# Performance work log

Hardware: AMD Instinct MI355X
Metric: run time of the kernel (lower is better)

The kernel has to match this reference:

```python
import jax, jax.numpy as jnp
import numpy as np

B, N, D, L = 64, 2047, 512, 4
T = D + 1        # token_dim = d + 1
H = 512          # hidden_dim
LN_EPS = 1e-5
ATTN_EPS = 1e-6


def setup_inputs() -> dict:
    key = jax.random.key(0)
    ks = jax.random.split(key, 10)
    s = 0.01  # matches xavier_uniform_ gain=0.01 small-init magnitude
    return dict(
        xs=jax.random.normal(ks[0], (B, N, D), jnp.float32),
        ys=jax.random.normal(ks[1], (B, N), jnp.float32),
        query_x=jax.random.normal(ks[2], (B, 1, D), jnp.float32),
        Wq=jax.random.normal(ks[3], (L, H, T), jnp.float32) * s,
        Wk=jax.random.normal(ks[4], (L, H, T), jnp.float32) * s,
        Wv=jax.random.normal(ks[5], (L, T, T), jnp.float32) * s,
        Wo=jax.random.normal(ks[6], (L, T, T), jnp.float32) * s,
        ln1_w=jnp.ones((L, T), jnp.float32),
        ln1_b=jnp.zeros((L, T), jnp.float32),
        ln2_w=jnp.ones((L, T), jnp.float32),
        ln2_b=jnp.zeros((L, T), jnp.float32),
        scale=jnp.ones((L,), jnp.float32),
        pred_w=jax.random.normal(ks[7], (1, T), jnp.float32) * 0.02,
    )


def _ln(x, w, b):
    m = jnp.mean(x, axis=-1, keepdims=True)
    v = jnp.var(x, axis=-1, keepdims=True)
    return (x - m) * jax.lax.rsqrt(v + LN_EPS) * w + b


def _l2norm(x):
    n = jnp.sqrt(jnp.sum(x * x, axis=-1, keepdims=True))
    return x / jnp.maximum(n, 1e-12)


def _forward(xs, ys, query_x, Wq, Wk, Wv, Wo, ln1_w, ln1_b, ln2_w, ln2_b, scale, pred_w):
    b = xs.shape[0]
    train_tokens = jnp.concatenate([xs, ys[..., None]], axis=-1)          # [B,N,T]
    query_token = jnp.concatenate([query_x, jnp.zeros((b, 1, 1), xs.dtype)], axis=-1)
    tokens = jnp.concatenate([train_tokens, query_token], axis=1)          # [B,N+1,T]

    def step(tok, p):
        wq, wk, wv, wo, w1, b1, w2, b2, sc = p
        x = _ln(tok, w1, b1)
        Q = jnp.einsum('bnt,ht->bnh', x, wq)
        K = jnp.einsum('bnt,ht->bnh', x, wk)
        V = jnp.einsum('bnt,ut->bnu', x, wv)
        Q = _l2norm(Q)
        K = _l2norm(K)
        s = jax.nn.softplus(sc)
        Qp = (jax.nn.elu(Q) + 1.0) * s
        Kp = jax.nn.elu(K) + 1.0
        KV = jnp.einsum('bnh,bnu->bhu', Kp, V)      # [B,H,T]
        Ksum = jnp.sum(Kp, axis=1)                  # [B,H]
        denom = jnp.einsum('bnh,bh->bn', Qp, Ksum)  # [B,N+1]
        attn = jnp.einsum('bnh,bhu->bnu', Qp, KV) / (denom[..., None] + ATTN_EPS)
        out = jnp.einsum('bnu,tu->bnt', attn, wo) * 0.1 + tok
        return _ln(out, w2, b2), None

    tokens, _ = jax.lax.scan(step, tokens, (Wq, Wk, Wv, Wo, ln1_w, ln1_b, ln2_w, ln2_b, scale))
    q_out = tokens[:, -1, :]                        # [B,T]
    return jnp.einsum('bt,ot->bo', q_out, pred_w)[..., 0]  # [B]


def reference(xs, ys, query_x, Wq, Wk, Wv, Wo, ln1_w, ln1_b, ln2_w, ln2_b, scale, pred_w):
    return _forward(xs, ys, query_x, Wq, Wk, Wv, Wo, ln1_w, ln1_b, ln2_w, ln2_b, scale, pred_w)
```

## Files before the change

kernel.cpp:

```cpp
#include <hip/hip_runtime.h>
#include <cstdint>
#include <cstddef>


typedef unsigned short u16;
typedef float f32x4 __attribute__((ext_vector_type(4)));
typedef unsigned short u16x8 __attribute__((ext_vector_type(8)));

#define P 576
#define NQK 1664
#define VTROWS 514
#define KVLD 640

__device__ __forceinline__ float bf2f(u16 s) {
    union { unsigned u; float f; } v; v.u = ((unsigned)s) << 16; return v.f;
}
__device__ __forceinline__ u16 f2bf(float f) {
    union { float f; unsigned u; } v; v.f = f;
    unsigned r = v.u + 0x7FFF + ((v.u >> 16) & 1);
    return (u16)(r >> 16);
}
__device__ __forceinline__ float wredsum(float v) {
#pragma unroll
    for (int o = 32; o > 0; o >>= 1) v += __shfl_xor(v, o, 64);
    return v;
}
__device__ __forceinline__ f32x4 mfma_16x16x32_bf16(u16x8 a, u16x8 b, f32x4 c) {
    asm volatile("v_mfma_f32_16x16x32_bf16 %0, %1, %2, %0"
                 : "+v"(c) : "v"(a), "v"(b));
    return c;
}
__device__ __forceinline__ void gload_lds16(const u16* g, u16* l) {
    __builtin_amdgcn_global_load_lds(
        (const __attribute__((address_space(1))) void*)g,
        (__attribute__((address_space(3))) void*)l, 16, 0, 0);
}

__global__ __launch_bounds__(256) void k_build_tokens(
    const float* __restrict__ xs, const float* __restrict__ ys,
    const float* __restrict__ qx, u16* __restrict__ tok,
    float* __restrict__ meanb, float* __restrict__ rstdb)
{
    long row = (long)blockIdx.x * 4 + (threadIdx.x >> 6);
    int lane = threadIdx.x & 63;
    int b = (int)(row >> 11), n = (int)(row & 2047);
    const float* src = (n < 2047) ? xs + ((long)(b * 2047 + n)) * 512
                                  : qx + (long)b * 512;
    float4 f0 = *(const float4*)(src + lane * 8);
    float4 f1 = *(const float4*)(src + lane * 8 + 4);
    float y = (n < 2047) ? ys[(long)b * 2047 + n] : 0.f;
    float v[8] = {f0.x, f0.y, f0.z, f0.w, f1.x, f1.y, f1.z, f1.w};
    float s = 0.f, sq = 0.f;
#pragma unroll
    for (int j = 0; j < 8; j++) { s += v[j]; sq += v[j] * v[j]; }
    if (lane == 0) { s += y; sq += y * y; }
    s = wredsum(s); sq = wredsum(sq);
    u16x8 o;
#pragma unroll
    for (int j = 0; j < 8; j++) o[j] = f2bf(v[j]);
    *(u16x8*)(tok + row * P + lane * 8) = o;
    if (lane < 8) {
        u16x8 z8 = {0,0,0,0,0,0,0,0};
        if (lane == 0) z8[0] = f2bf(y);
        *(u16x8*)(tok + row * P + 512 + lane * 8) = z8;
    }
    if (lane == 0) {
        float m = s * (1.f / 513.f);
        float var = sq * (1.f / 513.f) - m * m;
        meanb[row] = m;
        rstdb[row] = 1.f / sqrtf(var + 1e-5f);
    }
}

__global__ __launch_bounds__(256) void k_prep_wcat(
    const float* __restrict__ wq, const float* __restrict__ wk,
    const float* __restrict__ wv, const float* __restrict__ ln1w,
    u16* __restrict__ wcat)
{
    long idx = (long)blockIdx.x * 256 + threadIdx.x;
    if (idx >= 4L * NQK * P) return;
    int t = (int)(idx % P);
    long rem = idx / P;
    int r = (int)(rem % NQK);
    int l = (int)(rem / NQK);
    float v = 0.f;
    if (t < 513) {
        float wsc = ln1w[l * 513 + t];
        if (r < 512)       v = wq[((long)l * 512 + r) * 513 + t] * wsc;
        else if (r < 1024) v = wk[((long)l * 512 + (r - 512)) * 513 + t] * wsc;
        else if (r < 1537) v = wv[((long)l * 513 + (r - 1024)) * 513 + t] * wsc;
    }
    wcat[idx] = f2bf(v);
}

__global__ __launch_bounds__(256) void k_prep_wo(
    const float* __restrict__ wo, u16* __restrict__ wop)
{
    long idx = (long)blockIdx.x * 256 + threadIdx.x;
    if (idx >= 4L * P * P) return;
    int u = (int)(idx % P);
    long rem = idx / P;
    int t = (int)(rem % P);
    int l = (int)(rem / P);
    float v = (t < 513 && u < 513) ? wo[((long)l * 513 + t) * 513 + u] : 0.f;
    wop[idx] = f2bf(v);
}

__global__ __launch_bounds__(256) void k_prep_sums(
    const float* __restrict__ wq, const float* __restrict__ wk,
    const float* __restrict__ wv, const float* __restrict__ ln1w,
    const float* __restrict__ ln1b, float* __restrict__ s1, float* __restrict__ s2)
{
    int id = blockIdx.x * 4 + (threadIdx.x >> 6);
    int lane = threadIdx.x & 63;
    int l = id / NQK, r = id % NQK;
    float a1 = 0.f, a2 = 0.f;
    for (int t = lane; t < 513; t += 64) {
        float wc = 0.f;
        if (r < 512)       wc = wq[((long)l * 512 + r) * 513 + t];
        else if (r < 1024) wc = wk[((long)l * 512 + (r - 512)) * 513 + t];
        else if (r < 1537) wc = wv[((long)l * 513 + (r - 1024)) * 513 + t];
        a1 += ln1w[l * 513 + t] * wc;
        a2 += ln1b[l * 513 + t] * wc;
    }
    a1 = wredsum(a1); a2 = wredsum(a2);
    if (lane == 0) { s1[id] = a1; s2[id] = a2; }
}

__global__ __launch_bounds__(256) void k_ln2(
    const u16* __restrict__ z, u16* __restrict__ tok,
    const float* __restrict__ w, const float* __restrict__ bia,
    float* __restrict__ meanb, float* __restrict__ rstdb,
    const float* __restrict__ znum, const float* __restrict__ denomb)
{
    long row = (long)blockIdx.x * 4 + (threadIdx.x >> 6);
    int lane = threadIdx.x & 63;
    const u16* zp = z + row * P;
    u16* tp = tok + row * P;
    u16x8 a0 = *(const u16x8*)(zp + lane * 8);
    float zc = 0.f;
    if (lane == 0)
        zc = 0.1f * znum[row] / (denomb[row] + 1e-6f) + bf2f(tp[512]);
    float v0[8], v1[8];
#pragma unroll
    for (int j = 0; j < 8; j++) v0[j] = bf2f(a0[j]);
#pragma unroll
    for (int j = 0; j < 8; j++) v1[j] = 0.f;
    v1[0] = zc;
    float s = 0.f, sq = 0.f;
#pragma unroll
    for (int j = 0; j < 8; j++) { s += v0[j]; sq += v0[j] * v0[j]; }
#pragma unroll
    for (int j = 0; j < 8; j++) { s += v1[j]; sq += v1[j] * v1[j]; }
    s = wredsum(s); sq = wredsum(sq);
    float mean = s * (1.f / 513.f);
    float var = sq * (1.f / 513.f) - mean * mean;
    float rstd = 1.f / sqrtf(var + 1e-5f);
    float so = 0.f, so2 = 0.f;
    u16x8 o0;
    float of0[8];
#pragma unroll
    for (int j = 0; j < 8; j++) {
        int t = lane * 8 + j;
        of0[j] = (v0[j] - mean) * rstd * w[t] + bia[t];
        so += of0[j]; so2 += of0[j] * of0[j];
        o0[j] = f2bf(of0[j]);
    }
    float of1[8];
#pragma unroll
    for (int j = 0; j < 8; j++) {
        int t = 512 + lane * 8 + j;
        float ov = 0.f;
        if (lane < 8 && t < 513) ov = (v1[j] - mean) * rstd * w[t] + bia[t];
        of1[j] = ov;
        so += ov; so2 += ov * ov;
    }
    so = wredsum(so); so2 = wredsum(so2);
    *(u16x8*)(tp + lane * 8) = o0;
    if (lane < 8) {
        u16x8 o1;
#pragma unroll
        for (int j = 0; j < 8; j++) o1[j] = f2bf(of1[j]);
        *(u16x8*)(tp + 512 + lane * 8) = o1;
    }
    if (lane == 0) {
        float m2 = so * (1.f / 513.f);
        float v2 = so2 * (1.f / 513.f) - m2 * m2;
        meanb[row] = m2;
        rstdb[row] = 1.f / sqrtf(v2 + 1e-5f);
    }
}

__global__ __launch_bounds__(256) void k_qkt(
    u16* __restrict__ qkv, u16* __restrict__ kpt,
    float* __restrict__ ksum, float* __restrict__ v512sum,
    const u16* __restrict__ vt, const float* __restrict__ scale, int l)
{
    long row0 = (long)blockIdx.x * 64;
    int b = (int)(row0 >> 11);
    int nloc = (int)(row0 & 2047);
    int tid = threadIdx.x, lane = tid & 63, w = tid >> 6;
    float s = log1pf(expf(scale[l]));
    __shared__ u16 Kp[64][520];
    __shared__ u16 T2[64 * 80];

#pragma unroll 4
    for (int i = 0; i < 16; i++) {
        int rl = w * 16 + i;
        u16* rp = qkv + (row0 + rl) * NQK;
        u16x8 q8 = *(const u16x8*)(rp + lane * 8);
        u16x8 k8 = *(const u16x8*)(rp + 512 + lane * 8);
        float qf[8], kf[8];
        float sq = 0.f, sk = 0.f;
#pragma unroll
        for (int j = 0; j < 8; j++) { qf[j] = bf2f(q8[j]); sq += qf[j] * qf[j]; }
#pragma unroll
        for (int j = 0; j < 8; j++) { kf[j] = bf2f(k8[j]); sk += kf[j] * kf[j]; }
        sq = wredsum(sq); sk = wredsum(sk);
        float rnq = 1.f / fmaxf(sqrtf(sq), 1e-12f);
        float rnk = 1.f / fmaxf(sqrtf(sk), 1e-12f);
        u16x8 o, kk;
#pragma unroll
        for (int j = 0; j < 8; j++) {
            float q = qf[j] * rnq;
            float qp = (q > 0.f) ? (q + 1.f) : expf(q);
            o[j] = f2bf(qp * s);
            float kv = kf[j] * rnk;
            kv = (kv > 0.f) ? (kv + 1.f) : expf(kv);
            kk[j] = f2bf(kv);
        }
        *(u16x8*)(rp + lane * 8) = o;
        *(u16x8*)&Kp[rl][lane * 8] = kk;
    }
    __syncthreads();

    const u16* vrow = vt + ((long)b * VTROWS + 512) * 2048 + nloc + (tid & 3) * 16;
    u16x8 va = *(const u16x8*)vrow;
    u16x8 vb = *(const u16x8*)(vrow + 8);
    float vf[16];
#pragma unroll
    for (int j = 0; j < 8; j++) { vf[j] = bf2f(va[j]); vf[8 + j] = bf2f(vb[j]); }

    int r = tid >> 2;
    int c0 = (tid & 3) * 16;
    for (int ct = 0; ct < 8; ct++) {
        u16x8 a = *(const u16x8*)&Kp[r][ct * 64 + c0];
        u16x8 d = *(const u16x8*)&Kp[r][ct * 64 + c0 + 8];
#pragma unroll
        for (int j = 0; j < 8; j++) T2[(c0 + j) * 80 + r] = a[j];
#pragma unroll
        for (int j = 0; j < 8; j++) T2[(c0 + 8 + j) * 80 + r] = d[j];
        __syncthreads();
        u16x8 w0 = *(const u16x8*)&T2[r * 80 + c0];
        u16x8 w1 = *(const u16x8*)&T2[r * 80 + c0 + 8];
        u16* dst = kpt + ((long)(b * 512 + ct * 64 + r)) * 2048 + nloc + c0;
        *(u16x8*)dst = w0;
        *(u16x8*)(dst + 8) = w1;
        float part = 0.f, p2 = 0.f;
#pragma unroll
        for (int j = 0; j < 8; j++) {
            float k0 = bf2f(w0[j]), k1 = bf2f(w1[j]);
            part += k0 + k1;
            p2 += k0 * vf[j] + k1 * vf[8 + j];
        }
        part += __shfl_xor(part, 1, 64);
        part += __shfl_xor(part, 2, 64);
        p2 += __shfl_xor(p2, 1, 64);
        p2 += __shfl_xor(p2, 2, 64);
        if ((tid & 3) == 0) {
            atomicAdd(&ksum[(long)b * 512 + ct * 64 + r], part);
            atomicAdd(&v512sum[(long)b * 512 + ct * 64 + r], p2);
        }
        __syncthreads();
    }
}

__global__ __launch_bounds__(512) void k_v512(
    const float* __restrict__ v512sum, u16* __restrict__ kvh)
{
    int b = blockIdx.x, h = threadIdx.x;
    kvh[((long)b * 512 + h) * KVLD + 512] = f2bf(v512sum[(long)b * 512 + h]);
}

__global__ __launch_bounds__(256) void k_denom(
    const u16* __restrict__ qkv, const float* __restrict__ ksum,
    const u16* __restrict__ w2t, float* __restrict__ denom,
    float* __restrict__ znum)
{
    long row = (long)blockIdx.x * 4 + (threadIdx.x >> 6);
    int lane = threadIdx.x & 63;
    int b = (int)(row >> 11);
    u16x8 q = *(const u16x8*)(qkv + row * NQK + lane * 8);
    const float* ks = ksum + (long)b * 512 + lane * 8;
    u16x8 w8 = *(const u16x8*)(w2t + (long)b * 576 * 512 + 512 * 512 + lane * 8);
    float acc = 0.f, acc2 = 0.f;
#pragma unroll
    for (int j = 0; j < 8; j++) {
        float qf = bf2f(q[j]);
        acc += qf * ks[j];
        acc2 += qf * bf2f(w8[j]);
    }
    acc = wredsum(acc);
    acc2 = wredsum(acc2);
    if (lane == 0) { denom[row] = acc; znum[row] = acc2; }
}

__global__ void k_predict(const u16* __restrict__ tok, const float* __restrict__ pw,
                          float* __restrict__ out)
{
    int b = blockIdx.x;
    int lane = threadIdx.x;
    const u16* rp = tok + ((long)b * 2048 + 2047) * P;
    float acc = 0.f;
    for (int t = lane; t < 513; t += 64) acc += bf2f(rp[t]) * pw[t];
    acc = wredsum(acc);
    if (lane == 0) out[b] = acc;
}

__global__ __launch_bounds__(256) void k_gemm_bt(
    const u16* __restrict__ A, const u16* __restrict__ Bt, u16* __restrict__ C,
    int M, int N, int K, int lda, int ldb, int ldc,
    long sA, long sB, long sC,
    const float* __restrict__ aux1, const float* __restrict__ aux2,
    const float* __restrict__ aux3, const float* __restrict__ aux4,
    long sAux, const u16* __restrict__ Res,
    float cscale, int mode, int r1, int padw,
    int ntm, int ntn, int nbz,
    u16* __restrict__ VT, int vtbase)
{
    int G = ntm * ntn * nbz;
    int id = blockIdx.x;
    int lin = (id & 7) * (G >> 3) + (id >> 3);
    int per = ntm * ntn;
    int bz = lin / per;
    int rem = lin - bz * per;
    int mt = rem / ntn;
    int nt = rem - mt * ntn;
    int m0 = mt * 128, n0 = nt * 128;

    A += (long)bz * sA; Bt += (long)bz * sB; C += (long)bz * sC;
    int tid = threadIdx.x, lane = tid & 63, w = tid >> 6;
    int wr = w >> 1, wc = w & 1;
    __shared__ u16 ldsbuf[2 * 128 * 64];
    u16* Als = ldsbuf;
    u16* Bls = ldsbuf + 128 * 64;
    __shared__ float auxR0[128], auxR1[128], auxA1[128];
    __shared__ float auxC0[128], auxC1[128], auxB1[128];

    if (tid < 128) {
        int gr = m0 + tid; if (gr >= M) gr = M - 1;
        float r0v = cscale, r1v = 0.f, a1v = 0.f;
        if (mode == 1) {
            const float* d1 = aux1 + (long)bz * sAux;
            r0v = cscale / (d1[gr] + 1e-6f);
        } else if (mode == 3) { r0v = aux1[gr]; r1v = aux2[gr]; }
        if (r1) a1v = bf2f(A[(long)gr * lda + K]);
        auxR0[tid] = r0v; auxR1[tid] = r1v; auxA1[tid] = a1v;
    } else {
        int t = tid - 128;
        int gc = n0 + t; if (gc >= N) gc = N - 1;
        float c0v = 0.f, c1v = 0.f, b1v = 0.f;
        if (mode == 3) { c0v = aux3[gc]; c1v = aux4[gc]; }
        if (r1) b1v = bf2f(Bt[(long)gc * ldb + K]);
        auxC0[t] = c0v; auxC1[t] = c1v; auxB1[t] = b1v;
    }

    f32x4 acc[4][4];
#pragma unroll
    for (int m = 0; m < 4; m++)
#pragma unroll
        for (int n = 0; n < 4; n++) { acc[m][n][0]=0.f; acc[m][n][1]=0.f; acc[m][n][2]=0.f; acc[m][n][3]=0.f; }

    int srow = lane >> 3;
    int scol = (lane & 7) * 8;
    int scolsw = scol ^ (srow << 3);
    int swz = (lane & 7) << 3;

    for (int k0 = 0; k0 < K; k0 += 64) {
#pragma unroll
        for (int i = 0; i < 4; i++) {
            int rt = (w * 4 + i) * 8 + srow;
            int gr = m0 + rt; gr = (gr < M) ? gr : (M - 1);
            gload_lds16(A + (long)gr * lda + k0 + scolsw, &Als[(w * 4 + i) * 512]);
        }
#pragma unroll
        for (int i = 0; i < 4; i++) {
            int rt = (w * 4 + i) * 8 + srow;
            int gc = n0 + rt; gc = (gc < N) ? gc : (N - 1);
            gload_lds16(Bt + (long)gc * ldb + k0 + scolsw, &Bls[(w * 4 + i) * 512]);
        }
        __syncthreads();
#pragma unroll
        for (int ks = 0; ks < 2; ks++) {
            u16x8 af[4], bfv[4];
#pragma unroll
            for (int m = 0; m < 4; m++) {
                int row = wr * 64 + m * 16 + (lane & 15);
                af[m] = *(const u16x8*)&Als[row * 64 + ((ks * 32 + (lane >> 4) * 8) ^ swz)];
            }
#pragma unroll
            for (int n = 0; n < 4; n++) {
                int col = wc * 64 + n * 16 + (lane & 15);
                bfv[n] = *(const u16x8*)&Bls[col * 64 + ((ks * 32 + (lane >> 4) * 8) ^ swz)];
            }
#pragma unroll
            for (int m = 0; m < 4; m++)
#pragma unroll
                for (int n = 0; n < 4; n++)
                    acc[m][n] = mfma_16x16x32_bf16(af[m], bfv[n], acc[m][n]);
        }
        __syncthreads();
    }

    bool isvt = (VT != nullptr) && (n0 >= vtbase);

    if (Res) {
        const u16* Rp = Res + (long)bz * sC;
#pragma unroll
        for (int i = 0; i < 8; i++) {
            int lrow = i * 16 + (tid >> 4);
            int lcol = (tid & 15) * 8;
            long gr = m0 + lrow; if (gr > (long)M - 1) gr = M - 1;
            long gcol = (long)n0 + lcol;
            long mx = (long)ldc - 8; if (gcol > mx) gcol = mx;
            *(u16x8*)&ldsbuf[lrow * 128 + lcol] = *(const u16x8*)&Rp[gr * ldc + gcol];
        }
        __syncthreads();
    }

    asm volatile("s_nop 7\n\ts_nop 7" ::: );

    if (!isvt) {
#pragma unroll
        for (int m = 0; m < 4; m++) {
            int lrbase = wr * 64 + m * 16 + ((lane >> 4) << 2);
#pragma unroll
            for (int n = 0; n < 4; n++) {
                int lc = wc * 64 + n * 16 + (lane & 15);
                float c0v = auxC0[lc], c1v = auxC1[lc], b1v = auxB1[lc];
#pragma unroll
                for (int r = 0; r < 4; r++) {
                    int lr = lrbase + r;
                    float wv = acc[m][n][r] + auxA1[lr] * b1v;
                    float v;
                    if (mode == 3) v = auxR1[lr] * (wv - auxR0[lr] * c0v) + c1v;
                    else {
                        v = wv * auxR0[lr];
                        if (Res) v += bf2f(ldsbuf[lr * 128 + lc]);
                    }
                    ldsbuf[lr * 128 + lc] = f2bf(v);
                }
            }
        }
        __syncthreads();

        int lcol = (tid & 15) * 8;
        int gc0 = n0 + lcol;
        bool colok = padw || (gc0 + 8 <= N);
#pragma unroll
        for (int i = 0; i < 8; i++) {
            int lrow = i * 16 + (tid >> 4);
            int gr = m0 + lrow;
            if (gr < M && colok) {
                *(u16x8*)&C[(long)gr * ldc + gc0] = *(const u16x8*)&ldsbuf[lrow * 128 + lcol];
            }
        }
    } else {
        int u0 = n0 - vtbase;
        int b = m0 >> 11;
        int nloc = m0 & 2047;
#pragma unroll
        for (int m = 0; m < 4; m++) {
            int lrbase = wr * 64 + m * 16 + ((lane >> 4) << 2);
#pragma unroll
            for (int n = 0; n < 4; n++) {
                int lc = wc * 64 + n * 16 + (lane & 15);
                float c0v = auxC0[lc], c1v = auxC1[lc], b1v = auxB1[lc];
#pragma unroll
                for (int r = 0; r < 4; r++) {
                    int lr = lrbase + r;
                    float wv = acc[m][n][r] + auxA1[lr] * b1v;
                    float v = (mode == 3) ? (auxR1[lr] * (wv - auxR0[lr] * c0v) + c1v)
                                          : (wv * auxR0[lr]);
                    ldsbuf[lc * 128 + (lr ^ ((lc & 7) << 3))] = f2bf(v);
                }
            }
        }
        __syncthreads();

        int nc = (tid & 15) * 8;
        const u16x8 ones = {0x3F80,0x3F80,0x3F80,0x3F80,0x3F80,0x3F80,0x3F80,0x3F80};
#pragma unroll
        for (int i = 0; i < 8; i++) {
            int ur = i * 16 + (tid >> 4);
            int u = u0 + ur;
            if (u < VTROWS) {
                u16x8 vv;
                if (u == 513) vv = ones;
                else vv = *(const u16x8*)&ldsbuf[ur * 128 + (nc ^ ((ur & 7) << 3))];
                *(u16x8*)&VT[((long)b * VTROWS + u) * 2048 + nloc + nc] = vv;
            }
        }
    }
}

extern "C" void kernel_launch(void* const* d_in, const int* in_sizes, int n_in,
                              void* d_out, int out_size, void* d_ws, size_t ws_size,
                              hipStream_t stream)
{
    const float* xs    = (const float*)d_in[0];
    const float* ys    = (const float*)d_in[1];
    const float* qx    = (const float*)d_in[2];
    const float* Wq    = (const float*)d_in[3];
    const float* Wk    = (const float*)d_in[4];
    const float* Wv    = (const float*)d_in[5];
    const float* Wo    = (const float*)d_in[6];
    const float* ln1w  = (const float*)d_in[7];
    const float* ln1b  = (const float*)d_in[8];
    const float* ln2w  = (const float*)d_in[9];
    const float* ln2b  = (const float*)d_in[10];
    const float* scale = (const float*)d_in[11];
    const float* predw = (const float*)d_in[12];
    float* out = (float*)d_out;

    char* ws = (char*)d_ws;
    u16*   tok   = (u16*)(ws + 0L);
    u16*   buf1  = (u16*)(ws + 150994944L);
    u16*   qkv   = (u16*)(ws + 301989888L);
    u16*   kpt   = (u16*)(ws + 738197504L);
    u16*   kvh   = (u16*)(ws + 872415232L);
    float* denom = (float*)(ws + 914358272L);
    float* meanb = (float*)(ws + 914882560L);
    float* rstdb = (float*)(ws + 915406848L);
    float* ksum  = (float*)(ws + 915931136L);
    u16*   wcat  = (u16*)(ws + 916062208L);
    u16*   wop   = (u16*)(ws + 923729920L);
    float* s1    = (float*)(ws + 926384128L);
    float* s2    = (float*)(ws + 926410752L);
    float* v512s = (float*)(ws + 285736960L);
    float* znum  = (float*)(ws + 285868032L);
    u16*   w2t   = kpt;

    k_build_tokens<<<32768, 256, 0, stream>>>(xs, ys, qx, tok, meanb, rstdb);
    {
        long n1 = 4L * NQK * P;
        k_prep_wcat<<<(int)((n1 + 255) / 256), 256, 0, stream>>>(Wq, Wk, Wv, ln1w, wcat);
        long n2 = 4L * P * P;
        k_prep_wo<<<(int)((n2 + 255) / 256), 256, 0, stream>>>(Wo, wop);
        k_prep_sums<<<1664, 256, 0, stream>>>(Wq, Wk, Wv, ln1w, ln1b, s1, s2);
    }

    for (int l = 0; l < 4; l++) {
        hipMemsetAsync(ksum, 0, 64 * 512 * sizeof(float), stream);
        hipMemsetAsync(v512s, 0, 64 * 512 * sizeof(float), stream);
        k_gemm_bt<<<13312, 256, 0, stream>>>(tok, wcat + (long)l * NQK * P, qkv,
            131072, NQK, 512, P, P, NQK, 0, 0, 0,
            meanb, rstdb, s1 + l * NQK, s2 + l * NQK, 0, nullptr,
            1.f, 3, 1, 0, 1024, 13, 1,
            buf1, 1024);
        k_qkt<<<2048, 256, 0, stream>>>(qkv, kpt, ksum, v512s, buf1, scale, l);
        k_gemm_bt<<<1024, 256, 0, stream>>>(kpt, buf1, kvh,
            512, 512, 2048, 2048, 2048, KVLD,
            512L * 2048, (long)VTROWS * 2048, 512L * KVLD,
            nullptr, nullptr, nullptr, nullptr, 0, nullptr, 1.f, 0, 0, 1,
            4, 4, 64, nullptr, 1 << 30);
        k_v512<<<64, 512, 0, stream>>>(v512s, kvh);
        k_gemm_bt<<<1280, 256, 0, stream>>>(wop + (long)l * P * P, kvh, w2t,
            576, 512, 512, P, KVLD, 512,
            0, 512L * KVLD, 576L * 512,
            nullptr, nullptr, nullptr, nullptr, 0, nullptr, 1.f, 0, 1, 0,
            5, 4, 64, nullptr, 1 << 30);
        k_denom<<<32768, 256, 0, stream>>>(qkv, ksum, w2t, denom, znum);
        k_gemm_bt<<<4096, 256, 0, stream>>>(qkv, w2t, buf1,
            2048, 512, 512, NQK, 512, P,
            2048L * NQK, 576L * 512, 2048L * P,
            denom, nullptr, nullptr, nullptr, 2048, tok,
            0.1f, 1, 0, 0, 16, 4, 64, nullptr, 1 << 30);
        k_ln2<<<32768, 256, 0, stream>>>(buf1, tok, ln2w + l * 513, ln2b + l * 513,
                                         meanb, rstdb, znum, denom);
    }
    k_predict<<<64, 64, 0, stream>>>(tok, predw, out);
}
```

Baseline: 3.342 ms.

## Fuse attention-output GEMM with residual add and LayerNorm-2 in one kernel

Replaces the separate output GEMM (which wrote an intermediate buffer) and the per-row LN2 kernel with a single kernel. Each block computes a full 32-row by 512-column tile with MFMA, adds the residual, and runs both LayerNorm statistics passes in shared memory before writing tokens. This removes the intermediate buffer round-trip and one launch per layer. In exchange each block is narrow in M and reloads the whole weight tile, and uses large LDS, which may reduce occupancy.

New measurement: 3.620 ms. 8.3% more time.

```diff
diff --git a/kernel.cpp b/kernel.cpp
--- a/kernel.cpp
+++ b/kernel.cpp
@@ -127,70 +127,6 @@
     if (lane == 0) { s1[id] = a1; s2[id] = a2; }
 }
 
-__global__ __launch_bounds__(256) void k_ln2(
-    const u16* __restrict__ z, u16* __restrict__ tok,
-    const float* __restrict__ w, const float* __restrict__ bia,
-    float* __restrict__ meanb, float* __restrict__ rstdb,
-    const float* __restrict__ znum, const float* __restrict__ denomb)
-{
-    long row = (long)blockIdx.x * 4 + (threadIdx.x >> 6);
-    int lane = threadIdx.x & 63;
-    const u16* zp = z + row * P;
-    u16* tp = tok + row * P;
-    u16x8 a0 = *(const u16x8*)(zp + lane * 8);
-    float zc = 0.f;
-    if (lane == 0)
-        zc = 0.1f * znum[row] / (denomb[row] + 1e-6f) + bf2f(tp[512]);
-    float v0[8], v1[8];
-#pragma unroll
-    for (int j = 0; j < 8; j++) v0[j] = bf2f(a0[j]);
-#pragma unroll
-    for (int j = 0; j < 8; j++) v1[j] = 0.f;
-    v1[0] = zc;
-    float s = 0.f, sq = 0.f;
-#pragma unroll
-    for (int j = 0; j < 8; j++) { s += v0[j]; sq += v0[j] * v0[j]; }
-#pragma unroll
-    for (int j = 0; j < 8; j++) { s += v1[j]; sq += v1[j] * v1[j]; }
-    s = wredsum(s); sq = wredsum(sq);
-    float mean = s * (1.f / 513.f);
-    float var = sq * (1.f / 513.f) - mean * mean;
-    float rstd = 1.f / sqrtf(var + 1e-5f);
-    float so = 0.f, so2 = 0.f;
-    u16x8 o0;
-    float of0[8];
-#pragma unroll
-    for (int j = 0; j < 8; j++) {
-        int t = lane * 8 + j;
-        of0[j] = (v0[j] - mean) * rstd * w[t] + bia[t];
-        so += of0[j]; so2 += of0[j] * of0[j];
-        o0[j] = f2bf(of0[j]);
-    }
-    float of1[8];
-#pragma unroll
-    for (int j = 0; j < 8; j++) {
-        int t = 512 + lane * 8 + j;
-        float ov = 0.f;
-        if (lane < 8 && t < 513) ov = (v1[j] - mean) * rstd * w[t] + bia[t];
-        of1[j] = ov;
-        so += ov; so2 += ov * ov;
-    }
-    so = wredsum(so); so2 = wredsum(so2);
-    *(u16x8*)(tp + lane * 8) = o0;
-    if (lane < 8) {
-        u16x8 o1;
-#pragma unroll
-        for (int j = 0; j < 8; j++) o1[j] = f2bf(of1[j]);
-        *(u16x8*)(tp + 512 + lane * 8) = o1;
-    }
-    if (lane == 0) {
-        float m2 = so * (1.f / 513.f);
-        float v2 = so2 * (1.f / 513.f) - m2 * m2;
-        meanb[row] = m2;
-        rstdb[row] = 1.f / sqrtf(v2 + 1e-5f);
-    }
-}
-
 __global__ __launch_bounds__(256) void k_qkt(
     u16* __restrict__ qkv, u16* __restrict__ kpt,
     float* __restrict__ ksum, float* __restrict__ v512sum,
@@ -315,6 +251,190 @@
     for (int t = lane; t < 513; t += 64) acc += bf2f(rp[t]) * pw[t];
     acc = wredsum(acc);
     if (lane == 0) out[b] = acc;
+}
+
+__global__ __launch_bounds__(512) void k_zln(
+    const u16* __restrict__ Qp, const u16* __restrict__ W2,
+    u16* __restrict__ tok,
+    const float* __restrict__ denom, const float* __restrict__ znum,
+    const float* __restrict__ g2, const float* __restrict__ b2,
+    float* __restrict__ meanb, float* __restrict__ rstdb)
+{
+    int id = blockIdx.x;
+    int lin = (id & 7) * 512 + (id >> 3);
+    int bz = lin >> 6;
+    int mt = lin & 63;
+    long rowg0 = (long)bz * 2048 + mt * 32;
+    int tid = threadIdx.x, lane = tid & 63, w = tid >> 6;
+
+    __shared__ u16 S[34816];
+    __shared__ float dinv[32], zcs[32];
+    __shared__ float red[2][32][8];
+    __shared__ float mean32[32], rstd32[32];
+    __shared__ float gbuf[513], bbuf[513];
+
+    const u16* Ag = Qp + rowg0 * NQK;
+    const u16* Bg = W2 + (long)bz * 576 * 512;
+    u16* tokp = tok + rowg0 * P;
+
+    if (tid < 32) {
+        long rg = rowg0 + tid;
+        float d = 1.f / (denom[rg] + 1e-6f);
+        dinv[tid] = 0.1f * d;
+        zcs[tid] = 0.1f * znum[rg] * d + bf2f(tok[rg * P + 512]);
+    }
+    gbuf[tid] = g2[tid]; bbuf[tid] = b2[tid];
+    if (tid == 0) { gbuf[512] = g2[512]; bbuf[512] = b2[512]; }
+
+    f32x4 acc[2][4];
+#pragma unroll
+    for (int m = 0; m < 2; m++)
+#pragma unroll
+        for (int n = 0; n < 4; n++) { acc[m][n][0]=0.f; acc[m][n][1]=0.f; acc[m][n][2]=0.f; acc[m][n][3]=0.f; }
+
+    int srow = lane >> 3;
+    int colsw = ((lane & 7) << 3) ^ (srow << 3);
+    int swz = (lane & 7) << 3;
+
+    for (int k0 = 0; k0 < 512; k0 += 64) {
+#pragma unroll
+        for (int i = 0; i < 8; i++) {
+            int rt = (w * 8 + i) * 8 + srow;
+            gload_lds16(Bg + (long)rt * 512 + k0 + colsw, &S[2048 + (w * 8 + i) * 512]);
+        }
+        if (w < 4) {
+            int rt = w * 8 + srow;
+            gload_lds16(Ag + (long)rt * NQK + k0 + colsw, &S[w * 512]);
+        }
+        __syncthreads();
+#pragma unroll
+        for (int ks = 0; ks < 2; ks++) {
+            u16x8 af[2], bfv[4];
+#pragma unroll
+            for (int m = 0; m < 2; m++) {
+                int row = m * 16 + (lane & 15);
+                af[m] = *(const u16x8*)&S[row * 64 + ((ks * 32 + (lane >> 4) * 8) ^ swz)];
+            }
+#pragma unroll
+            for (int n = 0; n < 4; n++) {
+                int col = w * 64 + n * 16 + (lane & 15);
+                bfv[n] = *(const u16x8*)&S[2048 + col * 64 + ((ks * 32 + (lane >> 4) * 8) ^ swz)];
+            }
+#pragma unroll
+            for (int m = 0; m < 2; m++)
+#pragma unroll
+                for (int n = 0; n < 4; n++)
+                    acc[m][n] = mfma_16x16x32_bf16(af[m], bfv[n], acc[m][n]);
+        }
+        __syncthreads();
+    }
+
+    {
+        int rr = tid >> 4, cc = (tid & 15) * 32;
+        const u16* rp = tokp + (long)rr * P + cc;
+#pragma unroll
+        for (int j = 0; j < 4; j++)
+            *(u16x8*)&S[rr * 520 + cc + j * 8] = *(const u16x8*)(rp + j * 8);
+    }
+    __syncthreads();
+
+    float s8[2][4], q8[2][4];
+#pragma unroll
+    for (int m = 0; m < 2; m++)
+#pragma unroll
+    for (int r = 0; r < 4; r++) {
+        int row = m * 16 + ((lane >> 4) << 2) + r;
+        float s = 0.f, q = 0.f;
+#pragma unroll
+        for (int n = 0; n < 4; n++) {
+            int col = w * 64 + n * 16 + (lane & 15);
+            float v = acc[m][n][r] * dinv[row] + bf2f(S[row * 520 + col]);
+            s += v; q += v * v;
+        }
+        s8[m][r] = s; q8[m][r] = q;
+    }
+#pragma unroll
+    for (int m = 0; m < 2; m++)
+#pragma unroll
+    for (int r = 0; r < 4; r++) {
+#pragma unroll
+        for (int o = 8; o > 0; o >>= 1) {
+            s8[m][r] += __shfl_xor(s8[m][r], o, 64);
+            q8[m][r] += __shfl_xor(q8[m][r], o, 64);
+        }
+        if ((lane & 15) == 0) {
+            int row = m * 16 + ((lane >> 4) << 2) + r;
+            red[0][row][w] = s8[m][r];
+            red[1][row][w] = q8[m][r];
+        }
+    }
+    __syncthreads();
+    if (tid < 32) {
+        float zc = zcs[tid];
+        float s = zc, q = zc * zc;
+#pragma unroll
+        for (int ww = 0; ww < 8; ww++) { s += red[0][tid][ww]; q += red[1][tid][ww]; }
+        float mean = s * (1.f / 513.f);
+        float var = q * (1.f / 513.f) - mean * mean;
+        mean32[tid] = mean;
+        rstd32[tid] = 1.f / sqrtf(var + 1e-5f);
+    }
+    __syncthreads();
+
+#pragma unroll
+    for (int m = 0; m < 2; m++)
+#pragma unroll
+    for (int r = 0; r < 4; r++) {
+        int row = m * 16 + ((lane >> 4) << 2) + r;
+        float mean = mean32[row], rstd = rstd32[row], dv = dinv[row];
+        float s = 0.f, q = 0.f;
+#pragma unroll
+        for (int n = 0; n < 4; n++) {
+            int col = w * 64 + n * 16 + (lane & 15);
+            float v = acc[m][n][r] * dv + bf2f(S[row * 520 + col]);
+            float of = (v - mean) * rstd * gbuf[col] + bbuf[col];
+            s += of; q += of * of;
+            S[16640 + row * 520 + col] = f2bf(of);
+        }
+        s8[m][r] = s; q8[m][r] = q;
+    }
+#pragma unroll
+    for (int m = 0; m < 2; m++)
+#pragma unroll
+    for (int r = 0; r < 4; r++) {
+#pragma unroll
+        for (int o = 8; o > 0; o >>= 1) {
+            s8[m][r] += __shfl_xor(s8[m][r], o, 64);
+            q8[m][r] += __shfl_xor(q8[m][r], o, 64);
+        }
+        if ((lane & 15) == 0) {
+            int row = m * 16 + ((lane >> 4) << 2) + r;
+            red[0][row][w] = s8[m][r];
+            red[1][row][w] = q8[m][r];
+        }
+    }
+    __syncthreads();
+    if (tid < 32) {
+        long rg = rowg0 + tid;
+        float oc = (zcs[tid] - mean32[tid]) * rstd32[tid] * gbuf[512] + bbuf[512];
+        float s = oc, q = oc * oc;
+#pragma unroll
+        for (int ww = 0; ww < 8; ww++) { s += red[0][tid][ww]; q += red[1][tid][ww]; }
+        float m2 = s * (1.f / 513.f);
+        float v2 = q * (1.f / 513.f) - m2 * m2;
+        meanb[rg] = m2;
+        rstdb[rg] = 1.f / sqrtf(v2 + 1e-5f);
+        tok[rg * P + 512] = f2bf(oc);
+    }
+    __syncthreads();
+
+    {
+        int rr = tid >> 4, cc = (tid & 15) * 32;
+        u16* rp = tokp + (long)rr * P + cc;
+#pragma unroll
+        for (int j = 0; j < 4; j++)
+            *(u16x8*)(rp + j * 8) = *(const u16x8*)&S[16640 + rr * 520 + cc + j * 8];
+    }
 }
 
 __global__ __launch_bounds__(256) void k_gemm_bt(
@@ -571,13 +691,9 @@
             nullptr, nullptr, nullptr, nullptr, 0, nullptr, 1.f, 0, 1, 0,
             5, 4, 64, nullptr, 1 << 30);
         k_denom<<<32768, 256, 0, stream>>>(qkv, ksum, w2t, denom, znum);
-        k_gemm_bt<<<4096, 256, 0, stream>>>(qkv, w2t, buf1,
-            2048, 512, 512, NQK, 512, P,
-            2048L * NQK, 576L * 512, 2048L * P,
-            denom, nullptr, nullptr, nullptr, 2048, tok,
-            0.1f, 1, 0, 0, 16, 4, 64, nullptr, 1 << 30);
-        k_ln2<<<32768, 256, 0, stream>>>(buf1, tok, ln2w + l * 513, ln2b + l * 513,
-                                         meanb, rstdb, znum, denom);
+        k_zln<<<4096, 512, 0, stream>>>(qkv, w2t, tok, denom, znum,
+                                        ln2w + (long)l * 513, ln2b + (long)l * 513,
+                                        meanb, rstdb);
     }
     k_predict<<<64, 64, 0, stream>>>(tok, predw, out);
 }
```
